# Kernel optimization log

Hardware: AMD Instinct MI355X
Metric: run time of the kernel (lower is better)

Reference implementation:

```python
import jax, jax.numpy as jnp
import numpy as np

B, N, C, H, W = 32, 32, 3, 32, 32
HID, OUT = 256, 128


def _conv(x, w, b):
    y = jax.lax.conv_general_dilated(
        x, w, window_strides=(1, 1), padding="SAME",
        dimension_numbers=("NCHW", "OIHW", "NCHW"))
    return y + b[None, :, None, None]


def _sage(h, lw, lb, rw):
    # PyG SAGEConv with mean aggregation on a fully-connected graph (no self-loops):
    # agg_i = (sum_j h_j - h_i) / (N-1); out = agg @ lw.T + lb + h @ rw.T
    n = h.shape[1]
    agg = (jnp.sum(h, axis=1, keepdims=True) - h) / (n - 1)
    return jnp.einsum('bnd,od->bno', agg, lw) + lb + jnp.einsum('bnd,od->bno', h, rw)


def setup_inputs() -> dict:
    key = jax.random.key(0)
    ks = jax.random.split(key, 16)
    def g(k, shape, scale):
        return jax.random.normal(k, shape, dtype=jnp.float32) * scale
    return {
        "x": jax.random.normal(ks[0], (B, N, C, H, W), dtype=jnp.float32),
        "mask": jnp.ones((B, N), dtype=jnp.float32),
        "conv1_w": g(ks[1], (64, C, 3, 3), 0.1),
        "conv1_b": jnp.zeros((64,), jnp.float32),
        "conv2_w": g(ks[2], (128, 64, 3, 3), 0.05),
        "conv2_b": jnp.zeros((128,), jnp.float32),
        "fc_w": g(ks[3], (HID, 128), 0.08),
        "fc_b": jnp.zeros((HID,), jnp.float32),
        "s1_lw": g(ks[4], (HID, HID), 0.06),
        "s1_lb": jnp.zeros((HID,), jnp.float32),
        "s1_rw": g(ks[5], (HID, HID), 0.06),
        "s2_lw": g(ks[6], (OUT, HID), 0.06),
        "s2_lb": jnp.zeros((OUT,), jnp.float32),
        "s2_rw": g(ks[7], (OUT, HID), 0.06),
    }


def reference(x, mask, conv1_w, conv1_b, conv2_w, conv2_b, fc_w, fc_b,
              s1_lw, s1_lb, s1_rw, s2_lw, s2_lb, s2_rw):
    b, n, c, h, w = x.shape
    z = x.reshape(b * n, c, h, w)
    z = jax.nn.relu(_conv(z, conv1_w, conv1_b))
    z = jax.nn.relu(_conv(z, conv2_w, conv2_b))
    z = jnp.mean(z, axis=(2, 3))                      # AdaptiveAvgPool2d((1,1)) + flatten
    z = z @ fc_w.T + fc_b                             # [B*N, HID]
    z = z.reshape(b, n, -1) * mask[:, :, None]
    z = jax.nn.relu(_sage(z, s1_lw, s1_lb, s1_rw))
    z = _sage(z, s2_lw, s2_lb, s2_rw)                 # [B, N, OUT]
    return z
```

## Files before the change

### kernel.cpp

```cpp
#include <hip/hip_runtime.h>
#include <hip/hip_bf16.h>


typedef __attribute__((ext_vector_type(8))) short bfrag;
typedef __attribute__((ext_vector_type(4))) float f32x4;

static __device__ __forceinline__ unsigned short f2bf(float f) {
    union { float f; unsigned u; } v; v.f = f;
    unsigned r = v.u + 0x7fff + ((v.u >> 16) & 1);
    return (unsigned short)(r >> 16);
}

__global__ __launch_bounds__(256) void prep_kernel(
    const float* __restrict__ s1lw, const float* __restrict__ s1rw,
    const float* __restrict__ s2lw, const float* __restrict__ s2rw,
    const float* __restrict__ c2w, const float* __restrict__ c1w,
    const float* __restrict__ c1b, const float* __restrict__ fcw,
    float* __restrict__ l1T, float* __restrict__ w1pT,
    float* __restrict__ l2T, float* __restrict__ w2pT,
    float* __restrict__ fwT,
    short* __restrict__ w2b, short* __restrict__ w1b) {
    int i = blockIdx.x * 256 + threadIdx.x;
    const float inv31 = 1.f / 31.f;
    if (i < 65536) {
        int d = i >> 8, o = i & 255;
        float lw = s1lw[o * 256 + d];
        l1T[i]  = lw;
        w1pT[i] = s1rw[o * 256 + d] - lw * inv31;
    }
    if (i < 32768) {
        int d = i >> 7, o = i & 127;
        float lw = s2lw[o * 256 + d];
        l2T[i]  = lw;
        w2pT[i] = s2rw[o * 256 + d] - lw * inv31;
        int c = i >> 8, o2 = i & 255;
        fwT[i] = fcw[o2 * 128 + c];
    }
    if (i < 73728) {
        int k = i >> 13, rem = i & 8191, oc = rem >> 6, ic = rem & 63;
        w2b[i] = (short)f2bf(c2w[(oc * 64 + ic) * 9 + k]);
    }
    if (i < 2048) {
        int oc = i >> 5, k = i & 31;
        float v = (k < 27) ? c1w[oc * 27 + k] : (k == 27 ? c1b[oc] : 0.f);
        w1b[i] = (short)f2bf(v);
    }
}

__global__ __launch_bounds__(256, 2) void fused_conv_kernel(
    const float* __restrict__ x, const short* __restrict__ w1b,
    const short* __restrict__ w2b, const float* __restrict__ b2,
    float* __restrict__ pooled4) {
    const int band = blockIdx.x, img = blockIdx.y;
    __shared__ short xt[3 * 12 * 34];
    __shared__ short c1t[10 * 34 * 72];
    __shared__ float wsum[4][64];
    const int t = threadIdx.x;
    const int w = t >> 6, lane = t & 63;
    const int ln15 = lane & 15, q8 = (lane >> 4) * 8;
    const int rg2 = w & 1, og = w >> 1;

    const float* xi = x + img * 3072;
    for (int idx = t; idx < 1224; idx += 256) {
        int c = idx / 408, rem = idx % 408, r = rem / 34, col = rem % 34;
        int y = band * 8 - 2 + r, xx = col - 1;
        float v = 0.f;
        if ((unsigned)y < 32u && (unsigned)xx < 32u) v = xi[c * 1024 + y * 32 + xx];
        xt[idx] = (short)f2bf(v);
    }
    {
        f32x4 z = {0.f, 0.f, 0.f, 0.f};
        for (int i = t; i < 180; i += 256) {
            int r = i / 18, rem = i % 18, side = rem / 9, q = rem % 9;
            *(f32x4*)(c1t + (r * 34 + side * 33) * 72 + q * 8) = z;
        }
    }
    bfrag b1f[4];
#pragma unroll
    for (int ot = 0; ot < 4; ++ot)
        b1f[ot] = *(const bfrag*)(w1b + (ot * 16 + ln15) * 32 + q8);
    __syncthreads();

#pragma unroll 1
    for (int pt = 0; pt < 5; ++pt) {
        const int tile = w * 5 + pt;
        const int posA = tile * 16 + ln15;
        const int baseA = (posA >> 5) * 34 + (posA & 31);
        bfrag a1f;
#pragma unroll
        for (int j = 0; j < 8; ++j) {
            int k = q8 + j;
            int c = (k * 57) >> 9;
            int rem = k - 9 * c;
            int dy = (rem * 11) >> 5;
            int dx = rem - 3 * dy;
            int cc = c < 3 ? c : 2;
            short v = xt[cc * 408 + baseA + dy * 34 + dx];
            if (c >= 3) v = (k == 27) ? (short)0x3F80 : (short)0;
            a1f[j] = v;
        }
        f32x4 acc1[4];
#pragma unroll
        for (int ot = 0; ot < 4; ++ot) {
#pragma unroll
            for (int rg = 0; rg < 4; ++rg) acc1[ot][rg] = 0.f;
            acc1[ot] = __builtin_amdgcn_mfma_f32_16x16x32_bf16(
                a1f, b1f[ot], acc1[ot], 0, 0, 0);
        }
#pragma unroll
        for (int rg = 0; rg < 4; ++rg) {
            int pos = tile * 16 + (lane >> 4) * 4 + rg;
            int r = pos >> 5, xc = pos & 31;
            int y = band * 8 - 1 + r;
            bool valid = (unsigned)y < 32u;
#pragma unroll
            for (int ot = 0; ot < 4; ++ot) {
                float v = fmaxf(acc1[ot][rg], 0.f);
                c1t[(r * 34 + xc + 1) * 72 + ot * 16 + ln15] =
                    valid ? (short)f2bf(v) : (short)0;
            }
        }
    }
    __syncthreads();

    float b2v[4];
#pragma unroll
    for (int ot = 0; ot < 4; ++ot) b2v[ot] = b2[og * 64 + ot * 16 + ln15];

    f32x4 acc[8][4];
#pragma unroll
    for (int pt = 0; pt < 8; ++pt)
#pragma unroll
        for (int ot = 0; ot < 4; ++ot)
#pragma unroll
            for (int rg = 0; rg < 4; ++rg) acc[pt][ot][rg] = 0.f;

    int aBase[8];
#pragma unroll
    for (int pt = 0; pt < 8; ++pt) {
        int r = rg2 * 4 + (pt >> 1);
        int xc = ((pt & 1) << 4) + ln15;
        aBase[pt] = (r * 34 + xc) * 72 + q8;
    }

    const short* wb0 = w2b + (og * 64 + ln15) * 64 + q8;
    auto loadB = [&](bfrag* dst, int tap) {
        const short* p = wb0 + tap * 8192;
#pragma unroll
        for (int kc = 0; kc < 2; ++kc)
#pragma unroll
            for (int ot = 0; ot < 4; ++ot)
                dst[kc * 4 + ot] = *(const bfrag*)(p + ot * 1024 + kc * 32);
    };
    auto compute = [&](const bfrag* bf, int tap) {
        const int dy = tap / 3, dx = tap - dy * 3;
        const int dOff = (dy * 34 + dx) * 72;
#pragma unroll
        for (int pt = 0; pt < 8; ++pt) {
            const int a0 = aBase[pt] + dOff;
#pragma unroll
            for (int kc = 0; kc < 2; ++kc) {
                bfrag a2f = *(const bfrag*)(&c1t[a0 + kc * 32]);
#pragma unroll
                for (int ot = 0; ot < 4; ++ot)
                    acc[pt][ot] = __builtin_amdgcn_mfma_f32_16x16x32_bf16(
                        a2f, bf[kc * 4 + ot], acc[pt][ot], 0, 0, 0);
            }
        }
    };

    bfrag bA[8], bB[8];
    loadB(bA, 0);
#pragma unroll 1
    for (int tap = 0; tap < 9; tap += 2) {
        if (tap + 1 < 9) loadB(bB, tap + 1);
        compute(bA, tap);
        if (tap + 2 < 9) loadB(bA, tap + 2);
        if (tap + 1 < 9) compute(bB, tap + 1);
    }

#pragma unroll
    for (int ot = 0; ot < 4; ++ot) {
        float s = 0.f;
#pragma unroll
        for (int pt = 0; pt < 8; ++pt)
#pragma unroll
            for (int rg = 0; rg < 4; ++rg)
                s += fmaxf(acc[pt][ot][rg] + b2v[ot], 0.f);
        s += __shfl_xor(s, 16, 64);
        s += __shfl_xor(s, 32, 64);
        if (lane < 16) wsum[w][ot * 16 + ln15] = s;
    }
    __syncthreads();
    if (t < 128) {
        int og2 = t >> 6, oo = t & 63;
        pooled4[((size_t)img * 4 + band) * 128 + t] =
            wsum[og2 * 2][oo] + wsum[og2 * 2 + 1][oo];
    }
}

__global__ __launch_bounds__(256) void fc_kernel(
    const float* __restrict__ pooled4, const float* __restrict__ fwT,
    const float* __restrict__ fb, const float* __restrict__ mask,
    float* __restrict__ z1) {
    const int img = blockIdx.x;
    __shared__ float m[128];
    const int t = threadIdx.x;
    if (t < 128) {
        const float* p = pooled4 + (size_t)img * 4 * 128 + t;
        m[t] = (p[0] + p[128] + p[256] + p[384]) * (1.f / 1024.f);
    }
    __syncthreads();
    float acc = fb[t];
#pragma unroll 4
    for (int c = 0; c < 128; ++c) acc = fmaf(m[c], fwT[c * 256 + t], acc);
    z1[img * 256 + t] = acc * mask[img];
}

__global__ __launch_bounds__(256) void sage1_kernel(
    const float* __restrict__ z1, const float* __restrict__ l1T,
    const float* __restrict__ lb, const float* __restrict__ w1pT,
    float* __restrict__ z2) {
    const int bb = blockIdx.x >> 3, chunk = blockIdx.x & 7;
    __shared__ float h[32 * 256];
    __shared__ float sl[256];
    const int t = threadIdx.x;
    const float* zb = z1 + bb * 8192;
    for (int idx = t; idx < 8192; idx += 256) h[idx] = zb[idx];
    __syncthreads();
    float s = 0.f;
#pragma unroll
    for (int n = 0; n < 32; ++n) s += h[n * 256 + t];
    sl[t] = s * (1.f / 31.f);
    __syncthreads();
    float c = lb[t];
#pragma unroll 4
    for (int d = 0; d < 256; ++d) c = fmaf(sl[d], l1T[d * 256 + t], c);
    float acc[4];
#pragma unroll
    for (int i = 0; i < 4; ++i) acc[i] = c;
    for (int d0 = 0; d0 < 256; d0 += 4) {
        float wv0 = w1pT[(d0 + 0) * 256 + t];
        float wv1 = w1pT[(d0 + 1) * 256 + t];
        float wv2 = w1pT[(d0 + 2) * 256 + t];
        float wv3 = w1pT[(d0 + 3) * 256 + t];
#pragma unroll
        for (int i = 0; i < 4; ++i) {
            f32x4 hv = *(const f32x4*)&h[(chunk * 4 + i) * 256 + d0];
            acc[i] = fmaf(hv[0], wv0, acc[i]);
            acc[i] = fmaf(hv[1], wv1, acc[i]);
            acc[i] = fmaf(hv[2], wv2, acc[i]);
            acc[i] = fmaf(hv[3], wv3, acc[i]);
        }
    }
    for (int i = 0; i < 4; ++i)
        z2[(bb * 32 + chunk * 4 + i) * 256 + t] = fmaxf(acc[i], 0.f);
}

__global__ __launch_bounds__(256) void sage2_kernel(
    const float* __restrict__ z2, const float* __restrict__ l2T,
    const float* __restrict__ lb, const float* __restrict__ w2pT,
    float* __restrict__ out) {
    const int bb = blockIdx.x >> 3, chunk = blockIdx.x & 7;
    __shared__ float h[32 * 256];
    __shared__ float sl[256];
    const int t = threadIdx.x;
    const float* zb = z2 + bb * 8192;
    for (int idx = t; idx < 8192; idx += 256) h[idx] = zb[idx];
    __syncthreads();
    float s = 0.f;
#pragma unroll
    for (int n = 0; n < 32; ++n) s += h[n * 256 + t];
    sl[t] = s * (1.f / 31.f);
    __syncthreads();
    const int o = t & 127, half = t >> 7;
    float c = lb[o];
#pragma unroll 4
    for (int d = 0; d < 256; ++d) c = fmaf(sl[d], l2T[d * 128 + o], c);
    float acc[2];
    acc[0] = c; acc[1] = c;
    const int n0 = chunk * 4 + half * 2;
    for (int d0 = 0; d0 < 256; d0 += 4) {
        float wv0 = w2pT[(d0 + 0) * 128 + o];
        float wv1 = w2pT[(d0 + 1) * 128 + o];
        float wv2 = w2pT[(d0 + 2) * 128 + o];
        float wv3 = w2pT[(d0 + 3) * 128 + o];
#pragma unroll
        for (int ii = 0; ii < 2; ++ii) {
            f32x4 hv = *(const f32x4*)&h[(n0 + ii) * 256 + d0];
            acc[ii] = fmaf(hv[0], wv0, acc[ii]);
            acc[ii] = fmaf(hv[1], wv1, acc[ii]);
            acc[ii] = fmaf(hv[2], wv2, acc[ii]);
            acc[ii] = fmaf(hv[3], wv3, acc[ii]);
        }
    }
    for (int ii = 0; ii < 2; ++ii)
        out[(size_t)(bb * 32 + n0 + ii) * 128 + o] = acc[ii];
}

extern "C" void kernel_launch(void* const* d_in, const int* in_sizes, int n_in,
                              void* d_out, int out_size, void* d_ws, size_t ws_size,
                              hipStream_t stream) {
    const float* x    = (const float*)d_in[0];
    const float* mask = (const float*)d_in[1];
    const float* c1w  = (const float*)d_in[2];
    const float* c1b  = (const float*)d_in[3];
    const float* c2w  = (const float*)d_in[4];
    const float* c2b  = (const float*)d_in[5];
    const float* fcw  = (const float*)d_in[6];
    const float* fcb  = (const float*)d_in[7];
    const float* s1lw = (const float*)d_in[8];
    const float* s1lb = (const float*)d_in[9];
    const float* s1rw = (const float*)d_in[10];
    const float* s2lw = (const float*)d_in[11];
    const float* s2lb = (const float*)d_in[12];
    const float* s2rw = (const float*)d_in[13];
    float* out = (float*)d_out;

    char* ws = (char*)d_ws;
    float* pooled4 = (float*)(ws);
    float* z1      = (float*)(ws + 2048u * 1024);
    float* z2      = (float*)(ws + 3072u * 1024);
    float* l1T     = (float*)(ws + 4096u * 1024);
    float* w1pT    = (float*)(ws + 4352u * 1024);
    float* l2T     = (float*)(ws + 4608u * 1024);
    float* w2pT    = (float*)(ws + 4736u * 1024);
    float* fwT     = (float*)(ws + 4864u * 1024);
    short* w2b     = (short*)(ws + 4992u * 1024);
    short* w1b     = (short*)(ws + 5136u * 1024);

    prep_kernel<<<dim3(288), 256, 0, stream>>>(s1lw, s1rw, s2lw, s2rw, c2w, c1w, c1b,
                                               fcw, l1T, w1pT, l2T, w2pT, fwT, w2b, w1b);
    fused_conv_kernel<<<dim3(4, 1024), 256, 0, stream>>>(x, w1b, w2b, c2b, pooled4);
    fc_kernel<<<dim3(1024), 256, 0, stream>>>(pooled4, fwT, fcb, mask, z1);
    sage1_kernel<<<dim3(256), 256, 0, stream>>>(z1, l1T, s1lb, w1pT, z2);
    sage2_kernel<<<dim3(256), 256, 0, stream>>>(z2, l2T, s2lb, w2pT, out);
}
```

Before: 312.5 us.

## Switch conv2 to 32x32x16 MFMA with per-wave row tiling and repacked weights

Conv2 now runs on 32x32x16 bf16 MFMA instead of 16x16x32. Each wave owns two full output rows and all 128 output channels, and the weights are repacked in the prep kernel to match the new B-fragment layout. The K loop splits into 18 stages (tap by K half) with double-buffered A and B fragments. This raises MFMA work per fragment load and reduces B-operand global traffic per wave, at the cost of larger accumulators (128 floats per lane) and register pressure. Conv1 im2col index math is also hoisted out of the tile loop into precomputed offsets and masks.

```diff
diff --git a/kernel.cpp b/kernel.cpp
--- a/kernel.cpp
+++ b/kernel.cpp
@@ -4,6 +4,7 @@
 
 typedef __attribute__((ext_vector_type(8))) short bfrag;
 typedef __attribute__((ext_vector_type(4))) float f32x4;
+typedef __attribute__((ext_vector_type(16))) float f32x16;
 
 static __device__ __forceinline__ unsigned short f2bf(float f) {
     union { float f; unsigned u; } v; v.f = f;
@@ -19,7 +20,7 @@
     float* __restrict__ l1T, float* __restrict__ w1pT,
     float* __restrict__ l2T, float* __restrict__ w2pT,
     float* __restrict__ fwT,
-    short* __restrict__ w2b, short* __restrict__ w1b) {
+    short* __restrict__ w2c, short* __restrict__ w1b) {
     int i = blockIdx.x * 256 + threadIdx.x;
     const float inv31 = 1.f / 31.f;
     if (i < 65536) {
@@ -37,8 +38,10 @@
         fwT[i] = fcw[o2 * 128 + c];
     }
     if (i < 73728) {
-        int k = i >> 13, rem = i & 8191, oc = rem >> 6, ic = rem & 63;
-        w2b[i] = (short)f2bf(c2w[(oc * 64 + ic) * 9 + k]);
+        int tap = i >> 13, r = i & 8191;
+        int ks = r >> 11, hi = (r >> 10) & 1, oc = (r >> 3) & 127, j = i & 7;
+        int ic = ks * 16 + hi * 8 + j;
+        w2c[i] = (short)f2bf(c2w[(oc * 64 + ic) * 9 + tap]);
     }
     if (i < 2048) {
         int oc = i >> 5, k = i & 31;
@@ -49,16 +52,16 @@
 
 __global__ __launch_bounds__(256, 2) void fused_conv_kernel(
     const float* __restrict__ x, const short* __restrict__ w1b,
-    const short* __restrict__ w2b, const float* __restrict__ b2,
+    const short* __restrict__ w2c, const float* __restrict__ b2,
     float* __restrict__ pooled4) {
     const int band = blockIdx.x, img = blockIdx.y;
     __shared__ short xt[3 * 12 * 34];
     __shared__ short c1t[10 * 34 * 72];
-    __shared__ float wsum[4][64];
+    __shared__ float wsum[4][128];
     const int t = threadIdx.x;
     const int w = t >> 6, lane = t & 63;
     const int ln15 = lane & 15, q8 = (lane >> 4) * 8;
-    const int rg2 = w & 1, og = w >> 1;
+    const int ln31 = lane & 31, hi = lane >> 5;
 
     const float* xi = x + img * 3072;
     for (int idx = t; idx < 1224; idx += 256) {
@@ -79,6 +82,20 @@
 #pragma unroll
     for (int ot = 0; ot < 4; ++ot)
         b1f[ot] = *(const bfrag*)(w1b + (ot * 16 + ln15) * 32 + q8);
+
+    int xOff[8]; int kMask[8]; int kOvr[8];
+#pragma unroll
+    for (int j = 0; j < 8; ++j) {
+        int k = q8 + j;
+        int c = (k * 57) >> 9;
+        int rem = k - 9 * c;
+        int dy = (rem * 11) >> 5;
+        int dx = rem - 3 * dy;
+        int cc = c < 3 ? c : 2;
+        xOff[j] = cc * 408 + dy * 34 + dx;
+        kMask[j] = (c < 3) ? 0xFFFF : 0;
+        kOvr[j]  = (c < 3) ? 0 : (k == 27 ? 0x3F80 : 0);
+    }
     __syncthreads();
 
 #pragma unroll 1
@@ -88,17 +105,8 @@
         const int baseA = (posA >> 5) * 34 + (posA & 31);
         bfrag a1f;
 #pragma unroll
-        for (int j = 0; j < 8; ++j) {
-            int k = q8 + j;
-            int c = (k * 57) >> 9;
-            int rem = k - 9 * c;
-            int dy = (rem * 11) >> 5;
-            int dx = rem - 3 * dy;
-            int cc = c < 3 ? c : 2;
-            short v = xt[cc * 408 + baseA + dy * 34 + dx];
-            if (c >= 3) v = (k == 27) ? (short)0x3F80 : (short)0;
-            a1f[j] = v;
-        }
+        for (int j = 0; j < 8; ++j)
+            a1f[j] = (short)((xt[xOff[j] + baseA] & kMask[j]) | kOvr[j]);
         f32x4 acc1[4];
 #pragma unroll
         for (int ot = 0; ot < 4; ++ot) {
@@ -125,77 +133,71 @@
 
     float b2v[4];
 #pragma unroll
-    for (int ot = 0; ot < 4; ++ot) b2v[ot] = b2[og * 64 + ot * 16 + ln15];
-
-    f32x4 acc[8][4];
-#pragma unroll
-    for (int pt = 0; pt < 8; ++pt)
+    for (int ot = 0; ot < 4; ++ot) b2v[ot] = b2[ot * 32 + ln31];
+
+    f32x16 acc[2][4];
+#pragma unroll
+    for (int pt = 0; pt < 2; ++pt)
 #pragma unroll
         for (int ot = 0; ot < 4; ++ot)
 #pragma unroll
-            for (int rg = 0; rg < 4; ++rg) acc[pt][ot][rg] = 0.f;
-
-    int aBase[8];
-#pragma unroll
-    for (int pt = 0; pt < 8; ++pt) {
-        int r = rg2 * 4 + (pt >> 1);
-        int xc = ((pt & 1) << 4) + ln15;
-        aBase[pt] = (r * 34 + xc) * 72 + q8;
-    }
-
-    const short* wb0 = w2b + (og * 64 + ln15) * 64 + q8;
-    auto loadB = [&](bfrag* dst, int tap) {
-        const short* p = wb0 + tap * 8192;
-#pragma unroll
-        for (int kc = 0; kc < 2; ++kc)
+            for (int rg = 0; rg < 16; ++rg) acc[pt][ot][rg] = 0.f;
+
+    const int aB0 = (w * 2 * 34 + ln31) * 72 + hi * 8;
+    const int aB1 = aB0 + 34 * 72;
+    const short* bPtr = w2c + hi * 1024 + ln31 * 8;
+
+    bfrag aX[4], bX[8], aY[4], bY[8];
+    auto loadS = [&](bfrag* af, bfrag* bf, int st) {
+        const int tap = st >> 1, kh = st & 1;
+        const int dy = (tap * 11) >> 5, dx = tap - 3 * dy;
+        const int dOff = (dy * 34 + dx) * 72 + kh * 32;
+        af[0] = *(const bfrag*)&c1t[aB0 + dOff];
+        af[1] = *(const bfrag*)&c1t[aB0 + dOff + 16];
+        af[2] = *(const bfrag*)&c1t[aB1 + dOff];
+        af[3] = *(const bfrag*)&c1t[aB1 + dOff + 16];
+        const short* p = bPtr + st * 4096;
+#pragma unroll
+        for (int kk = 0; kk < 2; ++kk)
 #pragma unroll
             for (int ot = 0; ot < 4; ++ot)
-                dst[kc * 4 + ot] = *(const bfrag*)(p + ot * 1024 + kc * 32);
+                bf[kk * 4 + ot] = *(const bfrag*)(p + kk * 2048 + ot * 256);
     };
-    auto compute = [&](const bfrag* bf, int tap) {
-        const int dy = tap / 3, dx = tap - dy * 3;
-        const int dOff = (dy * 34 + dx) * 72;
-#pragma unroll
-        for (int pt = 0; pt < 8; ++pt) {
-            const int a0 = aBase[pt] + dOff;
-#pragma unroll
-            for (int kc = 0; kc < 2; ++kc) {
-                bfrag a2f = *(const bfrag*)(&c1t[a0 + kc * 32]);
+    auto computeS = [&](const bfrag* af, const bfrag* bf) {
+#pragma unroll
+        for (int kk = 0; kk < 2; ++kk)
+#pragma unroll
+            for (int pt = 0; pt < 2; ++pt)
 #pragma unroll
                 for (int ot = 0; ot < 4; ++ot)
-                    acc[pt][ot] = __builtin_amdgcn_mfma_f32_16x16x32_bf16(
-                        a2f, bf[kc * 4 + ot], acc[pt][ot], 0, 0, 0);
-            }
-        }
+                    acc[pt][ot] = __builtin_amdgcn_mfma_f32_32x32x16_bf16(
+                        af[pt * 2 + kk], bf[kk * 4 + ot], acc[pt][ot], 0, 0, 0);
     };
 
-    bfrag bA[8], bB[8];
-    loadB(bA, 0);
+    loadS(aX, bX, 0);
 #pragma unroll 1
-    for (int tap = 0; tap < 9; tap += 2) {
-        if (tap + 1 < 9) loadB(bB, tap + 1);
-        compute(bA, tap);
-        if (tap + 2 < 9) loadB(bA, tap + 2);
-        if (tap + 1 < 9) compute(bB, tap + 1);
+    for (int st = 0; st < 18; st += 2) {
+        loadS(aY, bY, st + 1);
+        computeS(aX, bX);
+        if (st + 2 < 18) loadS(aX, bX, st + 2);
+        computeS(aY, bY);
     }
 
 #pragma unroll
     for (int ot = 0; ot < 4; ++ot) {
         float s = 0.f;
 #pragma unroll
-        for (int pt = 0; pt < 8; ++pt)
-#pragma unroll
-            for (int rg = 0; rg < 4; ++rg)
+        for (int pt = 0; pt < 2; ++pt)
+#pragma unroll
+            for (int rg = 0; rg < 16; ++rg)
                 s += fmaxf(acc[pt][ot][rg] + b2v[ot], 0.f);
-        s += __shfl_xor(s, 16, 64);
         s += __shfl_xor(s, 32, 64);
-        if (lane < 16) wsum[w][ot * 16 + ln15] = s;
+        if (lane < 32) wsum[w][ot * 32 + ln31] = s;
     }
     __syncthreads();
     if (t < 128) {
-        int og2 = t >> 6, oo = t & 63;
         pooled4[((size_t)img * 4 + band) * 128 + t] =
-            wsum[og2 * 2][oo] + wsum[og2 * 2 + 1][oo];
+            wsum[0][t] + wsum[1][t] + wsum[2][t] + wsum[3][t];
     }
 }
 
@@ -326,12 +328,12 @@
     float* l2T     = (float*)(ws + 4608u * 1024);
     float* w2pT    = (float*)(ws + 4736u * 1024);
     float* fwT     = (float*)(ws + 4864u * 1024);
-    short* w2b     = (short*)(ws + 4992u * 1024);
+    short* w2c     = (short*)(ws + 4992u * 1024);
     short* w1b     = (short*)(ws + 5136u * 1024);
 
     prep_kernel<<<dim3(288), 256, 0, stream>>>(s1lw, s1rw, s2lw, s2rw, c2w, c1w, c1b,
-                                               fcw, l1T, w1pT, l2T, w2pT, fwT, w2b, w1b);
-    fused_conv_kernel<<<dim3(4, 1024), 256, 0, stream>>>(x, w1b, w2b, c2b, pooled4);
+                                               fcw, l1T, w1pT, l2T, w2pT, fwT, w2c, w1b);
+    fused_conv_kernel<<<dim3(4, 1024), 256, 0, stream>>>(x, w1b, w2c, c2b, pooled4);
     fc_kernel<<<dim3(1024), 256, 0, stream>>>(pooled4, fwT, fcb, mask, z1);
     sage1_kernel<<<dim3(256), 256, 0, stream>>>(z1, l1T, s1lb, w1pT, z2);
     sage2_kernel<<<dim3(256), 256, 0, stream>>>(z2, l2T, s2lb, w2pT, out);
```

Result: faster. 288.3 us (-7.7%).
